# Performance work log

Hardware: AMD Instinct MI355X
Metric: run time of the kernel (lower is better)

The kernel has to match this reference:

```python
import jax, jax.numpy as jnp
import numpy as np

B, C, H, W = 8, 512, 64, 64


def setup_inputs() -> dict:
    key = jax.random.key(0)
    ks = jax.random.split(key, 7)
    s = 1.0 / np.sqrt(C)  # conv2d default init scale
    return {
        "x": jax.random.normal(ks[0], (B, C, H, W), dtype=jnp.float32),
        "wq": jax.random.normal(ks[1], (C, C), dtype=jnp.float32) * s,
        "bq": jax.random.normal(ks[2], (C,), dtype=jnp.float32) * s,
        "wk": jax.random.normal(ks[3], (C, C), dtype=jnp.float32) * s,
        "bk": jax.random.normal(ks[4], (C,), dtype=jnp.float32) * s,
        "wv": jax.random.normal(ks[5], (C, C), dtype=jnp.float32) * s,
        "bv": jax.random.normal(ks[6], (C,), dtype=jnp.float32) * s,
    }


def reference(x, wq, bq, wk, bk, wv, bv):
    b, c, h, w = x.shape
    xf = x.reshape(b, c, h * w)  # (B, C, N)
    # 1x1 convs == per-pixel channel GEMMs
    q = jnp.einsum("oc,bcn->bon", wq, xf) + bq[None, :, None]
    k = jnp.einsum("oc,bcn->bon", wk, xf) + bk[None, :, None]
    v = jnp.einsum("oc,bcn->bon", wv, xf) + bv[None, :, None]
    # channel attention: (B, C, C), contraction over spatial N
    attn = jax.nn.softmax(jnp.einsum("bin,bjn->bij", q, k), axis=-1)
    out = jnp.einsum("bij,bjn->bin", attn, v)
    return out.reshape(b, c, h, w)
```

## Files before the change

### kernel.cpp

```cpp
#include <hip/hip_runtime.h>


typedef unsigned short u16;
typedef short v8s __attribute__((ext_vector_type(8)));
typedef float v4f __attribute__((ext_vector_type(4)));

#define B_ 8
#define C_ 512
#define N_ 4096

__device__ __forceinline__ u16 f2bf(float f) {
  unsigned int u = __builtin_bit_cast(unsigned int, f);
  u = u + 0x7fffu + ((u >> 16) & 1u);
  return (u16)(u >> 16);
}
__device__ __forceinline__ float bf2f(u16 h) {
  unsigned int u = ((unsigned int)h) << 16;
  return __builtin_bit_cast(float, u);
}
__device__ __forceinline__ void gld_lds16(const u16* g, u16* l) {
  __builtin_amdgcn_global_load_lds((__attribute__((address_space(1))) void*)(g),
                                   (__attribute__((address_space(3))) void*)(l),
                                   16, 0, 0);
}

template <bool SPLIT, int EPI, bool TRI>
__global__ __launch_bounds__(256) void gemm_bt(
    const u16* __restrict__ Ah, const u16* __restrict__ Al, long long sA_,
    const u16* __restrict__ Bh, const u16* __restrict__ Bl, long long sB_,
    int K, int Kc, int nsplit, int ldc,
    float* __restrict__ Cf, float* __restrict__ Cf2, u16* __restrict__ Ch,
    long long sC_, const float* __restrict__ rowbias) {
  constexpr int NB = SPLIT ? 4 : 2;
  __shared__ __attribute__((aligned(16))) u16 pool[2 * NB * 128 * 32];

  int b, ks, ty_, tx_;
  if (TRI) {
    int L = (int)blockIdx.z * 10 + (int)blockIdx.x;
    int cpx = (B_ * nsplit * 10) >> 3;
    int Ls = (L & 7) * cpx + (L >> 3);
    int t = Ls % 10, z = Ls / 10;
    b = z / nsplit;
    ks = z % nsplit;
    ty_ = (t < 4) ? 0 : (t < 7) ? 1 : (t < 9) ? 2 : 3;
    tx_ = t - ((ty_ == 0) ? 0 : (ty_ == 1) ? 3 : (ty_ == 2) ? 5 : 6);
  } else {
    b = blockIdx.z / nsplit;
    ks = blockIdx.z % nsplit;
    ty_ = blockIdx.y;
    tx_ = blockIdx.x;
  }
  int tid = threadIdx.x, lane = tid & 63, w = tid >> 6;
  const u16* pAh = Ah + (size_t)b * sA_ + (size_t)ty_ * 128 * K;
  const u16* pBh = Bh + (size_t)b * sB_ + (size_t)tx_ * 128 * K;
  const u16* pAl = SPLIT ? (Al + (size_t)b * sA_ + (size_t)ty_ * 128 * K) : pAh;
  const u16* pBl = SPLIT ? (Bl + (size_t)b * sB_ + (size_t)tx_ * 128 * K) : pBh;
  int wr = (w >> 1) * 64, wc = (w & 1) * 64;
  v4f acc[4][4] = {};

  int srow_off = lane >> 2;
  int gcol = ((lane & 3) ^ ((lane >> 3) & 3)) * 8;

  const u16* sbase;
  int bufsel;
  if (SPLIT) {
    sbase = (w == 0) ? pAh : (w == 1) ? pAl : (w == 2) ? pBh : pBl;
    bufsel = w;
  } else {
    sbase = (w < 2) ? pAh : pBh;
    bufsel = (w >> 1);
  }

  int kbeg = ks * Kc;
  int nIter = Kc >> 5;

  auto STAGE = [&](int pb, int k0) {
    u16* lds = pool + (pb * NB + bufsel) * (128 * 32);
    if constexpr (SPLIT) {
      for (int t = 0; t < 8; ++t)
        gld_lds16(sbase + (size_t)(t * 16 + srow_off) * K + k0 + gcol,
                  lds + t * 16 * 32);
    } else {
      int o = (w & 1) * 4;
      for (int t = 0; t < 4; ++t) {
        int s = o + t;
        gld_lds16(sbase + (size_t)(s * 16 + srow_off) * K + k0 + gcol,
                  lds + s * 16 * 32);
      }
    }
  };

  int r = lane & 15, q = lane >> 4;
  int sw = (q ^ ((r >> 1) & 3)) * 8;

  STAGE(0, kbeg);
  for (int it = 0; it < nIter; ++it) {
    int cur = it & 1;
    bool pf = (it + 1 < nIter);
    if (pf) {
      STAGE(cur ^ 1, kbeg + (it + 1) * 32);
      if constexpr (SPLIT)
        asm volatile("s_waitcnt vmcnt(8)" ::: "memory");
      else
        asm volatile("s_waitcnt vmcnt(4)" ::: "memory");
    } else {
      asm volatile("s_waitcnt vmcnt(0)" ::: "memory");
    }
    __builtin_amdgcn_s_barrier();
    __builtin_amdgcn_sched_barrier(0);

    const u16* base = pool + cur * NB * (128 * 32);
    const u16* A0s = base;
    const u16* A1s = base + 128 * 32;
    const u16* B0s = base + (SPLIT ? 2 : 1) * (128 * 32);
    const u16* B1s = base + 3 * (128 * 32);
    v8s a0[4], a1[4], b0[4], b1[4];
    for (int mt = 0; mt < 4; ++mt) {
      int off = (wr + mt * 16 + r) * 32 + sw;
      a0[mt] = *(const v8s*)(const void*)(A0s + off);
      if (SPLIT) a1[mt] = *(const v8s*)(const void*)(A1s + off);
    }
    for (int nt = 0; nt < 4; ++nt) {
      int off = (wc + nt * 16 + r) * 32 + sw;
      b0[nt] = *(const v8s*)(const void*)(B0s + off);
      if (SPLIT) b1[nt] = *(const v8s*)(const void*)(B1s + off);
    }
    for (int mt = 0; mt < 4; ++mt)
      for (int nt = 0; nt < 4; ++nt) {
        acc[mt][nt] = __builtin_amdgcn_mfma_f32_16x16x32_bf16(a0[mt], b0[nt], acc[mt][nt], 0, 0, 0);
        if (SPLIT) {
          acc[mt][nt] = __builtin_amdgcn_mfma_f32_16x16x32_bf16(a0[mt], b1[nt], acc[mt][nt], 0, 0, 0);
          acc[mt][nt] = __builtin_amdgcn_mfma_f32_16x16x32_bf16(a1[mt], b0[nt], acc[mt][nt], 0, 0, 0);
        }
      }
    asm volatile("" ::: "memory");
    __builtin_amdgcn_s_barrier();
    asm volatile("" ::: "memory");
  }

  float* dst = (EPI == 4 && (ks & 1)) ? Cf2 : Cf;
  for (int mt = 0; mt < 4; ++mt)
    for (int nt = 0; nt < 4; ++nt) {
      int row0 = ty_ * 128 + wr + mt * 16 + q * 4;
      int col = tx_ * 128 + wc + nt * 16 + r;
      for (int e = 0; e < 4; ++e) {
        float vv = acc[mt][nt][e];
        size_t off = (size_t)b * sC_ + (size_t)(row0 + e) * ldc + col;
        if (EPI == 2) {
          Ch[off] = f2bf(vv);
        } else if (EPI == 3) {
          Cf[off] = vv + rowbias[(size_t)b * C_ + row0 + e];
        } else {
          atomicAdd(&dst[off], vv);
        }
      }
    }
}

__global__ __launch_bounds__(256) void conv_split_g(
    const float* __restrict__ A0, const float* __restrict__ A1,
    u16* __restrict__ h, u16* __restrict__ l) {
  size_t i = ((size_t)blockIdx.x * 256 + threadIdx.x) * 4;
  int b = (int)(i >> 18);
  int r = (int)(i >> 9) & 511;
  int c = (int)i & 511;
  size_t base = (size_t)b << 18;
  float v[4];
  if ((r >> 7) <= (c >> 7)) {
    const float* p0 = A0 + base + (size_t)r * C_ + c;
    const float* p1 = A1 + base + (size_t)r * C_ + c;
    float4 x0 = *(const float4*)p0;
    float4 x1 = *(const float4*)p1;
    v[0] = x0.x + x1.x; v[1] = x0.y + x1.y; v[2] = x0.z + x1.z; v[3] = x0.w + x1.w;
  } else {
    for (int j = 0; j < 4; ++j) {
      size_t s = base + (size_t)(c + j) * C_ + r;
      v[j] = A0[s] + A1[s];
    }
  }
  for (int j = 0; j < 4; ++j) {
    u16 hh = f2bf(v[j]);
    h[i + j] = hh;
    l[i + j] = f2bf(v[j] - bf2f(hh));
  }
}

__global__ __launch_bounds__(256) void conv_split(
    const float* __restrict__ acc, u16* __restrict__ h, u16* __restrict__ l,
    float* __restrict__ zbuf) {
  size_t i = (size_t)blockIdx.x * 256 + threadIdx.x;
  zbuf[i] = 0.0f;
  float v = acc[i];
  u16 hh = f2bf(v);
  h[i] = hh;
  l[i] = f2bf(v - bf2f(hh));
}

__global__ __launch_bounds__(256) void split_transpose(
    const float* __restrict__ x, u16* __restrict__ xh, u16* __restrict__ xl,
    u16* __restrict__ xhT, float* __restrict__ sx, float* __restrict__ accz) {
  __shared__ u16 tile[64 * 66];
  int b = blockIdx.z, ct = blockIdx.y, nt = blockIdx.x;
  int tid = threadIdx.x;
  {
    size_t zi = (size_t)((blockIdx.z * 8 + blockIdx.y) * 64 + blockIdx.x) * 256 + tid;
    ((float4*)accz)[zi] = make_float4(0.f, 0.f, 0.f, 0.f);
  }
  const float* xb = x + ((size_t)b * C_ + (size_t)ct * 64) * N_ + (size_t)nt * 64;
  for (int it = 0; it < 4; ++it) {
    int idx = it * 1024 + tid * 4;
    int cl = idx >> 6;
    int nl = idx & 63;
    float4 v = *(const float4*)(xb + (size_t)cl * N_ + nl);
    float vv[4] = {v.x, v.y, v.z, v.w};
    u16 h4[4], l4[4];
    for (int j = 0; j < 4; ++j) {
      h4[j] = f2bf(vv[j]);
      l4[j] = f2bf(vv[j] - bf2f(h4[j]));
    }
    size_t go = ((size_t)b * C_ + ct * 64 + cl) * N_ + (size_t)nt * 64 + nl;
    *(ushort4*)(xh + go) = make_ushort4(h4[0], h4[1], h4[2], h4[3]);
    *(ushort4*)(xl + go) = make_ushort4(l4[0], l4[1], l4[2], l4[3]);
    for (int j = 0; j < 4; ++j) tile[(nl + j) * 66 + cl] = h4[j];
    float s = vv[0] + vv[1] + vv[2] + vv[3];
    s += __shfl_xor(s, 1); s += __shfl_xor(s, 2);
    s += __shfl_xor(s, 4); s += __shfl_xor(s, 8);
    if ((tid & 15) == 0) atomicAdd(&sx[b * C_ + ct * 64 + cl], s);
  }
  __syncthreads();
  for (int it = 0; it < 4; ++it) {
    int idx = it * 1024 + tid * 4;
    int nr = idx >> 6;
    int c4 = idx & 63;
    const u16* tp = tile + nr * 66 + c4;
    unsigned int lo = *(const unsigned int*)(const void*)(tp);
    unsigned int hi = *(const unsigned int*)(const void*)(tp + 2);
    size_t to = ((size_t)b * N_ + (size_t)nt * 64 + nr) * C_ + ct * 64 + c4;
    *(ushort4*)(xhT + to) = make_ushort4((u16)lo, (u16)(lo >> 16), (u16)hi, (u16)(hi >> 16));
  }
}

__global__ __launch_bounds__(256) void prep_weights(
    const float* __restrict__ wq, const float* __restrict__ wk, const float* __restrict__ wv,
    u16* __restrict__ wqh, u16* __restrict__ wql, u16* __restrict__ wkh,
    u16* __restrict__ wkl, u16* __restrict__ wvT, float* __restrict__ sx) {
  int idx = blockIdx.x * 256 + threadIdx.x;
  if (blockIdx.x < 16) sx[idx] = 0.0f;
  float q = wq[idx];
  u16 qh = f2bf(q);
  wqh[idx] = qh;
  wql[idx] = f2bf(q - bf2f(qh));
  float k = wk[idx];
  u16 kh = f2bf(k);
  wkh[idx] = kh;
  wkl[idx] = f2bf(k - bf2f(kh));
  float v = wv[idx];
  wvT[(size_t)(idx & 511) * C_ + (idx >> 9)] = f2bf(v);
}

__global__ __launch_bounds__(256) void bias_vec(
    const float* __restrict__ wq, const float* __restrict__ wk,
    const float* __restrict__ sx, float* __restrict__ aq, float* __restrict__ ak) {
  int gw = blockIdx.x * 4 + (threadIdx.x >> 6);
  int lane = threadIdx.x & 63;
  int which = gw >> 12;
  int b = (gw >> 9) & 7, i = gw & 511;
  const float* wrow = (which ? wk : wq) + (size_t)i * C_;
  const float* sxb = sx + b * C_;
  float s = 0.f;
  for (int c = lane; c < C_; c += 64) s += wrow[c] * sxb[c];
  for (int o = 32; o; o >>= 1) s += __shfl_down(s, o);
  if (lane == 0) (which ? ak : aq)[b * C_ + i] = s;
}

__global__ __launch_bounds__(256) void softmax_rows(
    const float* __restrict__ Sraw, const float* __restrict__ aq,
    const float* __restrict__ ak, const float* __restrict__ bq,
    const float* __restrict__ bk, const float* __restrict__ bv,
    u16* __restrict__ attn, float* __restrict__ obias) {
  int row = blockIdx.x * 4 + (threadIdx.x >> 6);
  int lane = threadIdx.x & 63;
  int b = row >> 9, i = row & 511;
  const float* srow = Sraw + (size_t)row * C_;
  const float* akb = ak + b * C_;
  float aqi = aq[row], bqi = bq[i];
  float lv[8], ev[8];
  float m = -3.4e38f;
  for (int t = 0; t < 8; ++t) {
    int j = t * 64 + lane;
    float v = srow[j] + aqi * bk[j] + bqi * (akb[j] + 4096.0f * bk[j]);
    lv[t] = v;
    m = fmaxf(m, v);
  }
  for (int o = 32; o; o >>= 1) m = fmaxf(m, __shfl_xor(m, o));
  float se = 0.f, sb = 0.f;
  for (int t = 0; t < 8; ++t) {
    int j = t * 64 + lane;
    float e = expf(lv[t] - m);
    ev[t] = e;
    se += e;
    sb += e * bv[j];
  }
  for (int o = 32; o; o >>= 1) {
    se += __shfl_xor(se, o);
    sb += __shfl_xor(sb, o);
  }
  float inv = 1.0f / se;
  for (int t = 0; t < 8; ++t) attn[(size_t)row * C_ + t * 64 + lane] = f2bf(ev[t] * inv);
  if (lane == 0) obias[row] = sb * inv;
}

extern "C" void kernel_launch(void* const* d_in, const int* in_sizes, int n_in,
                              void* d_out, int out_size, void* d_ws, size_t ws_size,
                              hipStream_t stream) {
  const float* x = (const float*)d_in[0];
  const float* wq = (const float*)d_in[1];
  const float* bq = (const float*)d_in[2];
  const float* wk = (const float*)d_in[3];
  const float* bk = (const float*)d_in[4];
  const float* wv = (const float*)d_in[5];
  const float* bv = (const float*)d_in[6];
  float* out = (float*)d_out;

  const size_t XN = (size_t)B_ * C_ * N_;
  const size_t CCt = (size_t)B_ * C_ * C_;
  const size_t W2 = (size_t)C_ * C_;

  u16* XH = (u16*)d_ws;
  u16* XL = XH + XN;
  u16* XHT = XL + XN;
  float* ACC = (float*)(XHT + XN);
  float* ACC2 = ACC + CCt;
  u16* GH = (u16*)(ACC2 + CCt);
  u16* GL = GH + CCt;
  u16* UH = GL + CCt;
  u16* UL = UH + CCt;
  u16* ATTN = UL + CCt;
  u16* MH = ATTN + CCt;
  u16* WQH = MH + CCt;
  u16* WQL = WQH + W2;
  u16* WKH = WQL + W2;
  u16* WKL = WKH + W2;
  u16* WVT = WKL + W2;
  float* SX = (float*)(WVT + W2);
  float* AQ = SX + B_ * C_;
  float* AK = AQ + B_ * C_;
  float* OBIAS = AK + B_ * C_;

  prep_weights<<<W2 / 256, 256, 0, stream>>>(wq, wk, wv, WQH, WQL, WKH, WKL, WVT, SX);
  split_transpose<<<dim3(N_ / 64, C_ / 64, B_), 256, 0, stream>>>(x, XH, XL, XHT, SX, ACC);
  bias_vec<<<2048, 256, 0, stream>>>(wq, wk, SX, AQ, AK);

  gemm_bt<true, 4, true><<<dim3(10, 1, B_ * 8), 256, 0, stream>>>(
      XH, XL, (long long)((size_t)C_ * N_), XH, XL, (long long)((size_t)C_ * N_),
      N_, 512, 8, C_, ACC, ACC2, nullptr, (long long)W2, nullptr);
  conv_split_g<<<CCt / 1024, 256, 0, stream>>>(ACC, ACC2, GH, GL);

  hipMemsetAsync(ACC, 0, CCt * sizeof(float), stream);
  gemm_bt<true, 4, false><<<dim3(4, 4, B_ * 4), 256, 0, stream>>>(
      WKH, WKL, 0, GH, GL, (long long)W2, C_, 128, 4, C_, ACC, ACC, nullptr,
      (long long)W2, nullptr);
  conv_split<<<CCt / 256, 256, 0, stream>>>(ACC, UH, UL, ACC2);

  gemm_bt<true, 4, false><<<dim3(4, 4, B_ * 4), 256, 0, stream>>>(
      WQH, WQL, 0, UH, UL, (long long)W2, C_, 128, 4, C_, ACC2, ACC2, nullptr,
      (long long)W2, nullptr);

  softmax_rows<<<(B_ * C_) / 4, 256, 0, stream>>>(ACC2, AQ, AK, bq, bk, bv, ATTN, OBIAS);

  gemm_bt<false, 2, false><<<dim3(4, 4, B_), 256, 0, stream>>>(
      ATTN, nullptr, (long long)W2, WVT, nullptr, 0, C_, 512, 1, C_, nullptr, nullptr,
      MH, (long long)W2, nullptr);
  gemm_bt<false, 3, false><<<dim3(N_ / 128, 4, B_), 256, 0, stream>>>(
      MH, nullptr, (long long)W2, XHT, nullptr, (long long)((size_t)N_ * C_),
      C_, 512, 1, N_, out, nullptr, nullptr, (long long)((size_t)C_ * N_), OBIAS);
}
```

Baseline: 333.3 us.

## Replace atomic split-K accumulation with per-split partial buffers reduced downstream

Split-K GEMMs now write each split's 128x128 tile to its own slot in a partial buffer with plain stores, replacing atomicAdd into zeroed accumulators. The following conversion and softmax kernels sum the partials themselves, so the memset and in-kernel zeroing go away. This removes atomic contention and the zero-fill traffic. In exchange the reduction passes read several times more data (8 or 4 partials per element), and the Gram transpose path now does strided reads across the split slices.

```diff
diff --git a/kernel.cpp b/kernel.cpp
--- a/kernel.cpp
+++ b/kernel.cpp
@@ -29,12 +29,12 @@
     const u16* __restrict__ Ah, const u16* __restrict__ Al, long long sA_,
     const u16* __restrict__ Bh, const u16* __restrict__ Bl, long long sB_,
     int K, int Kc, int nsplit, int ldc,
-    float* __restrict__ Cf, float* __restrict__ Cf2, u16* __restrict__ Ch,
+    float* __restrict__ Cf, u16* __restrict__ Ch,
     long long sC_, const float* __restrict__ rowbias) {
   constexpr int NB = SPLIT ? 4 : 2;
   __shared__ __attribute__((aligned(16))) u16 pool[2 * NB * 128 * 32];
 
-  int b, ks, ty_, tx_;
+  int b, ks, ty_, tx_, tidx;
   if (TRI) {
     int L = (int)blockIdx.z * 10 + (int)blockIdx.x;
     int cpx = (B_ * nsplit * 10) >> 3;
@@ -42,6 +42,7 @@
     int t = Ls % 10, z = Ls / 10;
     b = z / nsplit;
     ks = z % nsplit;
+    tidx = t;
     ty_ = (t < 4) ? 0 : (t < 7) ? 1 : (t < 9) ? 2 : 3;
     tx_ = t - ((ty_ == 0) ? 0 : (ty_ == 1) ? 3 : (ty_ == 2) ? 5 : 6);
   } else {
@@ -49,6 +50,7 @@
     ks = blockIdx.z % nsplit;
     ty_ = blockIdx.y;
     tx_ = blockIdx.x;
+    tidx = ty_ * 4 + tx_;
   }
   int tid = threadIdx.x, lane = tid & 63, w = tid >> 6;
   const u16* pAh = Ah + (size_t)b * sA_ + (size_t)ty_ * 128 * K;
@@ -138,45 +140,56 @@
     asm volatile("" ::: "memory");
   }
 
-  float* dst = (EPI == 4 && (ks & 1)) ? Cf2 : Cf;
-  for (int mt = 0; mt < 4; ++mt)
-    for (int nt = 0; nt < 4; ++nt) {
-      int row0 = ty_ * 128 + wr + mt * 16 + q * 4;
-      int col = tx_ * 128 + wc + nt * 16 + r;
-      for (int e = 0; e < 4; ++e) {
-        float vv = acc[mt][nt][e];
-        size_t off = (size_t)b * sC_ + (size_t)(row0 + e) * ldc + col;
-        if (EPI == 2) {
-          Ch[off] = f2bf(vv);
-        } else if (EPI == 3) {
-          Cf[off] = vv + rowbias[(size_t)b * C_ + row0 + e];
-        } else {
-          atomicAdd(&dst[off], vv);
+  if (EPI == 4) {
+    constexpr int NT = TRI ? 10 : 16;
+    float* dstp = Cf + ((size_t)(b * nsplit + ks) * NT + tidx) * 16384;
+    for (int mt = 0; mt < 4; ++mt)
+      for (int nt = 0; nt < 4; ++nt) {
+        int rl = wr + mt * 16 + q * 4;
+        int cl = wc + nt * 16 + r;
+        for (int e = 0; e < 4; ++e)
+          dstp[(size_t)(rl + e) * 128 + cl] = acc[mt][nt][e];
+      }
+  } else {
+    for (int mt = 0; mt < 4; ++mt)
+      for (int nt = 0; nt < 4; ++nt) {
+        int row0 = ty_ * 128 + wr + mt * 16 + q * 4;
+        int col = tx_ * 128 + wc + nt * 16 + r;
+        for (int e = 0; e < 4; ++e) {
+          float vv = acc[mt][nt][e];
+          size_t off = (size_t)b * sC_ + (size_t)(row0 + e) * ldc + col;
+          if (EPI == 2) {
+            Ch[off] = f2bf(vv);
+          } else {
+            Cf[off] = vv + rowbias[(size_t)b * C_ + row0 + e];
+          }
         }
       }
-    }
+  }
 }
 
 __global__ __launch_bounds__(256) void conv_split_g(
-    const float* __restrict__ A0, const float* __restrict__ A1,
-    u16* __restrict__ h, u16* __restrict__ l) {
+    const float* __restrict__ P, u16* __restrict__ h, u16* __restrict__ l) {
   size_t i = ((size_t)blockIdx.x * 256 + threadIdx.x) * 4;
   int b = (int)(i >> 18);
   int r = (int)(i >> 9) & 511;
   int c = (int)i & 511;
-  size_t base = (size_t)b << 18;
-  float v[4];
-  if ((r >> 7) <= (c >> 7)) {
-    const float* p0 = A0 + base + (size_t)r * C_ + c;
-    const float* p1 = A1 + base + (size_t)r * C_ + c;
-    float4 x0 = *(const float4*)p0;
-    float4 x1 = *(const float4*)p1;
-    v[0] = x0.x + x1.x; v[1] = x0.y + x1.y; v[2] = x0.z + x1.z; v[3] = x0.w + x1.w;
+  int rq = r >> 7, cq = c >> 7;
+  float v[4] = {0.f, 0.f, 0.f, 0.f};
+  if (rq <= cq) {
+    int t = (rq == 0) ? cq : (rq == 1) ? 3 + cq : (rq == 2) ? 5 + cq : 6 + cq;
+    const float* p = P + ((size_t)(b * 8) * 10 + t) * 16384 +
+                     (size_t)(r & 127) * 128 + (c & 127);
+    for (int ks = 0; ks < 8; ++ks) {
+      float4 x0 = *(const float4*)(p + (size_t)ks * 10 * 16384);
+      v[0] += x0.x; v[1] += x0.y; v[2] += x0.z; v[3] += x0.w;
+    }
   } else {
-    for (int j = 0; j < 4; ++j) {
-      size_t s = base + (size_t)(c + j) * C_ + r;
-      v[j] = A0[s] + A1[s];
-    }
+    int t = (cq == 0) ? rq : (cq == 1) ? 3 + rq : (cq == 2) ? 5 + rq : 6 + rq;
+    const float* p = P + ((size_t)(b * 8) * 10 + t) * 16384 + (r & 127);
+    for (int j = 0; j < 4; ++j)
+      for (int ks = 0; ks < 8; ++ks)
+        v[j] += p[(size_t)ks * 10 * 16384 + (size_t)((c & 127) + j) * 128];
   }
   for (int j = 0; j < 4; ++j) {
     u16 hh = f2bf(v[j]);
@@ -186,26 +199,32 @@
 }
 
 __global__ __launch_bounds__(256) void conv_split(
-    const float* __restrict__ acc, u16* __restrict__ h, u16* __restrict__ l,
-    float* __restrict__ zbuf) {
-  size_t i = (size_t)blockIdx.x * 256 + threadIdx.x;
-  zbuf[i] = 0.0f;
-  float v = acc[i];
-  u16 hh = f2bf(v);
-  h[i] = hh;
-  l[i] = f2bf(v - bf2f(hh));
+    const float* __restrict__ P, u16* __restrict__ h, u16* __restrict__ l) {
+  size_t i = ((size_t)blockIdx.x * 256 + threadIdx.x) * 4;
+  int b = (int)(i >> 18);
+  int r = (int)(i >> 9) & 511;
+  int c = (int)i & 511;
+  int t = (r >> 7) * 4 + (c >> 7);
+  const float* p = P + ((size_t)(b * 4) * 16 + t) * 16384 +
+                   (size_t)(r & 127) * 128 + (c & 127);
+  float v[4] = {0.f, 0.f, 0.f, 0.f};
+  for (int ks = 0; ks < 4; ++ks) {
+    float4 x0 = *(const float4*)(p + (size_t)ks * 16 * 16384);
+    v[0] += x0.x; v[1] += x0.y; v[2] += x0.z; v[3] += x0.w;
+  }
+  for (int j = 0; j < 4; ++j) {
+    u16 hh = f2bf(v[j]);
+    h[i + j] = hh;
+    l[i + j] = f2bf(v[j] - bf2f(hh));
+  }
 }
 
 __global__ __launch_bounds__(256) void split_transpose(
     const float* __restrict__ x, u16* __restrict__ xh, u16* __restrict__ xl,
-    u16* __restrict__ xhT, float* __restrict__ sx, float* __restrict__ accz) {
+    u16* __restrict__ xhT, float* __restrict__ sx) {
   __shared__ u16 tile[64 * 66];
   int b = blockIdx.z, ct = blockIdx.y, nt = blockIdx.x;
   int tid = threadIdx.x;
-  {
-    size_t zi = (size_t)((blockIdx.z * 8 + blockIdx.y) * 64 + blockIdx.x) * 256 + tid;
-    ((float4*)accz)[zi] = make_float4(0.f, 0.f, 0.f, 0.f);
-  }
   const float* xb = x + ((size_t)b * C_ + (size_t)ct * 64) * N_ + (size_t)nt * 64;
   for (int it = 0; it < 4; ++it) {
     int idx = it * 1024 + tid * 4;
@@ -274,21 +293,25 @@
 }
 
 __global__ __launch_bounds__(256) void softmax_rows(
-    const float* __restrict__ Sraw, const float* __restrict__ aq,
+    const float* __restrict__ P, const float* __restrict__ aq,
     const float* __restrict__ ak, const float* __restrict__ bq,
     const float* __restrict__ bk, const float* __restrict__ bv,
     u16* __restrict__ attn, float* __restrict__ obias) {
   int row = blockIdx.x * 4 + (threadIdx.x >> 6);
   int lane = threadIdx.x & 63;
   int b = row >> 9, i = row & 511;
-  const float* srow = Sraw + (size_t)row * C_;
   const float* akb = ak + b * C_;
   float aqi = aq[row], bqi = bq[i];
   float lv[8], ev[8];
   float m = -3.4e38f;
   for (int t = 0; t < 8; ++t) {
     int j = t * 64 + lane;
-    float v = srow[j] + aqi * bk[j] + bqi * (akb[j] + 4096.0f * bk[j]);
+    int tile = (i >> 7) * 4 + (t >> 1);
+    size_t base = ((size_t)(b * 4) * 16 + tile) * 16384 +
+                  (size_t)(i & 127) * 128 + ((t & 1) * 64 + lane);
+    float sv = 0.f;
+    for (int ks = 0; ks < 4; ++ks) sv += P[base + (size_t)ks * 16 * 16384];
+    float v = sv + aqi * bk[j] + bqi * (akb[j] + 4096.0f * bk[j]);
     lv[t] = v;
     m = fmaxf(m, v);
   }
@@ -325,13 +348,13 @@
   const size_t XN = (size_t)B_ * C_ * N_;
   const size_t CCt = (size_t)B_ * C_ * C_;
   const size_t W2 = (size_t)C_ * C_;
+  const size_t PARTN = (size_t)B_ * 8 * 10 * 16384;
 
   u16* XH = (u16*)d_ws;
   u16* XL = XH + XN;
   u16* XHT = XL + XN;
-  float* ACC = (float*)(XHT + XN);
-  float* ACC2 = ACC + CCt;
-  u16* GH = (u16*)(ACC2 + CCt);
+  float* PART = (float*)(XHT + XN);
+  u16* GH = (u16*)(PART + PARTN);
   u16* GL = GH + CCt;
   u16* UH = GL + CCt;
   u16* UL = UH + CCt;
@@ -348,30 +371,29 @@
   float* OBIAS = AK + B_ * C_;
 
   prep_weights<<<W2 / 256, 256, 0, stream>>>(wq, wk, wv, WQH, WQL, WKH, WKL, WVT, SX);
-  split_transpose<<<dim3(N_ / 64, C_ / 64, B_), 256, 0, stream>>>(x, XH, XL, XHT, SX, ACC);
+  split_transpose<<<dim3(N_ / 64, C_ / 64, B_), 256, 0, stream>>>(x, XH, XL, XHT, SX);
   bias_vec<<<2048, 256, 0, stream>>>(wq, wk, SX, AQ, AK);
 
   gemm_bt<true, 4, true><<<dim3(10, 1, B_ * 8), 256, 0, stream>>>(
       XH, XL, (long long)((size_t)C_ * N_), XH, XL, (long long)((size_t)C_ * N_),
-      N_, 512, 8, C_, ACC, ACC2, nullptr, (long long)W2, nullptr);
-  conv_split_g<<<CCt / 1024, 256, 0, stream>>>(ACC, ACC2, GH, GL);
-
-  hipMemsetAsync(ACC, 0, CCt * sizeof(float), stream);
+      N_, 512, 8, C_, PART, nullptr, (long long)W2, nullptr);
+  conv_split_g<<<CCt / 1024, 256, 0, stream>>>(PART, GH, GL);
+
   gemm_bt<true, 4, false><<<dim3(4, 4, B_ * 4), 256, 0, stream>>>(
-      WKH, WKL, 0, GH, GL, (long long)W2, C_, 128, 4, C_, ACC, ACC, nullptr,
+      WKH, WKL, 0, GH, GL, (long long)W2, C_, 128, 4, C_, PART, nullptr,
       (long long)W2, nullptr);
-  conv_split<<<CCt / 256, 256, 0, stream>>>(ACC, UH, UL, ACC2);
+  conv_split<<<CCt / 1024, 256, 0, stream>>>(PART, UH, UL);
 
   gemm_bt<true, 4, false><<<dim3(4, 4, B_ * 4), 256, 0, stream>>>(
-      WQH, WQL, 0, UH, UL, (long long)W2, C_, 128, 4, C_, ACC2, ACC2, nullptr,
+      WQH, WQL, 0, UH, UL, (long long)W2, C_, 128, 4, C_, PART, nullptr,
       (long long)W2, nullptr);
 
-  softmax_rows<<<(B_ * C_) / 4, 256, 0, stream>>>(ACC2, AQ, AK, bq, bk, bv, ATTN, OBIAS);
+  softmax_rows<<<(B_ * C_) / 4, 256, 0, stream>>>(PART, AQ, AK, bq, bk, bv, ATTN, OBIAS);
 
   gemm_bt<false, 2, false><<<dim3(4, 4, B_), 256, 0, stream>>>(
-      ATTN, nullptr, (long long)W2, WVT, nullptr, 0, C_, 512, 1, C_, nullptr, nullptr,
+      ATTN, nullptr, (long long)W2, WVT, nullptr, 0, C_, 512, 1, C_, nullptr,
       MH, (long long)W2, nullptr);
   gemm_bt<false, 3, false><<<dim3(N_ / 128, 4, B_), 256, 0, stream>>>(
       MH, nullptr, (long long)W2, XHT, nullptr, (long long)((size_t)N_ * C_),
-      C_, 512, 1, N_, out, nullptr, nullptr, (long long)((size_t)C_ * N_), OBIAS);
-}
+      C_, 512, 1, N_, out, nullptr, (long long)((size_t)C_ * N_), OBIAS);
+}
```

After: 336.8 us. About the same (+1.1%).
